# Optimization experiments

Hardware: AMD Instinct MI355X
Metric: run time of the kernel (lower is better)

The kernel has to match this reference:

```python
import jax, jax.numpy as jnp
import numpy as np

N_HEAD = 16
MASKED_BIAS = -10000.0


def setup_inputs() -> dict:
    key = jax.random.key(0)
    k1, k2, k3 = jax.random.split(key, 3)
    B, S, D = 2, 2048, 1024
    scale_in = 0.02  # GPT-2 style init scale for weights
    return {
        "hidden_states": jax.random.normal(k1, (B, S, D), dtype=jnp.float32),
        "c_attn_w": jax.random.normal(k2, (D, 3 * D), dtype=jnp.float32) * scale_in,
        "c_attn_b": jnp.zeros((3 * D,), dtype=jnp.float32),
        "c_proj_w": jax.random.normal(k3, (D, D), dtype=jnp.float32) * scale_in,
        "c_proj_b": jnp.zeros((D,), dtype=jnp.float32),
    }


def reference(hidden_states, c_attn_w, c_attn_b, c_proj_w, c_proj_b):
    B, S, D = hidden_states.shape
    H = N_HEAD
    hd = D // H

    # Conv1D (HF): x @ W + b, fused QKV
    qkv = hidden_states @ c_attn_w + c_attn_b          # [B, S, 3D]
    q, k, v = jnp.split(qkv, 3, axis=-1)

    def to_heads(x):  # [B, S, D] -> [B, H, S, hd]
        return x.reshape(B, S, H, hd).transpose(0, 2, 1, 3)

    q, k, v = to_heads(q), to_heads(k), to_heads(v)

    # scaled scores (scale=True divides by sqrt(head_dim))
    w = jnp.einsum("bhqd,bhkd->bhqk", q, k) / jnp.float32(hd) ** 0.5  # [B,H,S,S]

    # causal mask via torch.where(mask, w, masked_bias)
    causal = jnp.tril(jnp.ones((S, S), dtype=bool))
    w = jnp.where(causal, w, jnp.float32(MASKED_BIAS))

    w = jax.nn.softmax(w, axis=-1)
    # attn_dropout / resid_dropout are identity in eval mode

    out = jnp.einsum("bhqk,bhkd->bhqd", w, v)          # [B,H,S,hd]
    out = out.transpose(0, 2, 1, 3).reshape(B, S, D)   # merge heads

    return out @ c_proj_w + c_proj_b                   # [B,S,D]
```

## Files before the change

kernel.cpp:

```cpp
#include <hip/hip_runtime.h>
#include <hip/hip_bf16.h>

typedef __attribute__((ext_vector_type(8))) short bf16x8;
typedef __attribute__((ext_vector_type(4))) float f32x4;
typedef __attribute__((ext_vector_type(4))) unsigned u32x4;

#define B_SZ 2
#define S_SZ 2048
#define D_SZ 1024
#define H_SZ 16
#define HD_SZ 64

static __device__ __forceinline__ short f2bf(float f) {
    unsigned u = __builtin_bit_cast(unsigned, f);
    u += 0x7FFFu + ((u >> 16) & 1u);
    return (short)(u >> 16);
}

static __device__ __forceinline__ float fexp2(float x) {
    float r; asm("v_exp_f32 %0, %1" : "=v"(r) : "v"(x)); return r;
}

static __device__ __forceinline__ unsigned cvtpk(float lo, float hi) {
    unsigned r; asm("v_cvt_pk_bf16_f32 %0, %1, %2" : "=v"(r) : "v"(lo), "v"(hi)); return r;
}

static __device__ __forceinline__ void gload16(const short* g, short* l) {
    __builtin_amdgcn_global_load_lds(
        (const __attribute__((address_space(1))) unsigned*)g,
        (__attribute__((address_space(3))) unsigned*)l,
        16, 0, 0);
}

#define SBAR() do { __builtin_amdgcn_sched_barrier(0); \
                    __builtin_amdgcn_s_barrier(); \
                    __builtin_amdgcn_sched_barrier(0); } while (0)

__global__ __launch_bounds__(256) void k_prep(const float* __restrict__ hs, short* __restrict__ Xb,
                                              const float* __restrict__ w1, short* __restrict__ W1T,
                                              const float* __restrict__ w2, short* __restrict__ W2T) {
    __shared__ float tile[32][33];
    const int id = blockIdx.x;
    const int tid = threadIdx.x;
    if (id < 4096) {
        int i = (id * 256 + tid) * 4;
        float4 v = *reinterpret_cast<const float4*>(hs + i);
        short4 o;
        o.x = f2bf(v.x); o.y = f2bf(v.y); o.z = f2bf(v.z); o.w = f2bf(v.w);
        *reinterpret_cast<short4*>(Xb + i) = o;
        return;
    }
    const float* in;
    short* out;
    int N, bx, by;
    if (id < 7168) {
        int bid = id - 4096;
        in = w1; out = W1T; N = 3072;
        bx = bid % 96; by = bid / 96;
    } else {
        int bid = id - 7168;
        in = w2; out = W2T; N = 1024;
        bx = bid & 31; by = bid >> 5;
    }
    const int k0 = by * 32, n0 = bx * 32;
    const int tx = tid & 31, ty = tid >> 5;
    #pragma unroll
    for (int i = 0; i < 4; ++i)
        tile[ty + i * 8][tx] = in[(size_t)(k0 + ty + i * 8) * N + n0 + tx];
    __syncthreads();
    #pragma unroll
    for (int i = 0; i < 4; ++i)
        out[(size_t)(n0 + ty + i * 8) * 1024 + k0 + tx] = f2bf(tile[tx][ty + i * 8]);
}

__global__ __launch_bounds__(512, 1) void k_gemm_qkv8(
    const short* __restrict__ A, const short* __restrict__ Bt,
    const float* __restrict__ bias,
    short* __restrict__ Qo, short* __restrict__ Ko, short* __restrict__ VTo) {
    constexpr int K = 1024, NT = 16;
    __shared__ short As[2][256 * 64];
    __shared__ short Bs[2][192 * 64];
    const int tid = threadIdx.x;
    const int lane = tid & 63;
    const int w = tid >> 6;
    const int wr = w >> 2, wc = w & 3;
    const int lr = lane & 15, lc = lane >> 4;
    const int bid = blockIdx.x;
    const int xcd = bid & 7, local = bid >> 3;
    const int bm = (xcd >> 1) * 4 + (local >> 3);
    const int bn = (xcd & 1) * 8 + (local & 7);
    const size_t arow0 = (size_t)bm * 256;
    const size_t brow0 = (size_t)bn * 192;

    const int srl = tid >> 3;
    const int sc8 = (tid & 7) ^ (srl & 7);
    const int dcol = (tid & 7) * 8;

    f32x4 acc[8][3];
    #pragma unroll
    for (int m = 0; m < 8; ++m)
        #pragma unroll
        for (int n = 0; n < 3; ++n)
            acc[m][n] = (f32x4){0.f, 0.f, 0.f, 0.f};

    auto STAGE_A = [&](int T) {
        const int buf = T & 1;
        #pragma unroll
        for (int j = 0; j < 4; ++j) {
            int row = j * 64 + srl;
            gload16(&A[(arow0 + row) * K + T * 64 + sc8 * 8], &As[buf][row * 64 + dcol]);
        }
    };
    auto STAGE_B = [&](int T) {
        const int buf = T & 1;
        #pragma unroll
        for (int j = 0; j < 3; ++j) {
            int row = j * 64 + srl;
            gload16(&Bt[(brow0 + row) * K + T * 64 + sc8 * 8], &Bs[buf][row * 64 + dcol]);
        }
    };

    const int rx = (lr & 7) * 8;
    auto LDA = [&](int buf, int rowoff, int c) {
        return *reinterpret_cast<const bf16x8*>(
            &As[buf][(wr * 128 + rowoff + lr) * 64 + (((c * 32) + lc * 8) ^ rx)]);
    };
    auto LDB = [&](int buf, int n, int c) {
        return *reinterpret_cast<const bf16x8*>(
            &Bs[buf][(wc * 48 + n * 16 + lr) * 64 + (((c * 32) + lc * 8) ^ rx)]);
    };

    bf16x8 at[4][2];
    bf16x8 bfr[3][2];

    STAGE_A(0); STAGE_B(0); STAGE_B(1);
    asm volatile("s_waitcnt vmcnt(3)" ::: "memory");
    SBAR();

    for (int T = 0; T < NT; ++T) {
        const int buf = T & 1;
        #pragma unroll
        for (int m = 0; m < 4; ++m)
            #pragma unroll
            for (int c = 0; c < 2; ++c)
                at[m][c] = LDA(buf, m * 16, c);
        #pragma unroll
        for (int n = 0; n < 3; ++n)
            #pragma unroll
            for (int c = 0; c < 2; ++c)
                bfr[n][c] = LDB(buf, n, c);
        if (T + 1 < NT) STAGE_A(T + 1);
        SBAR();
        __builtin_amdgcn_s_setprio(1);
        #pragma unroll
        for (int m = 0; m < 4; ++m)
            #pragma unroll
            for (int n = 0; n < 3; ++n)
                #pragma unroll
                for (int c = 0; c < 2; ++c)
                    acc[m][n] = __builtin_amdgcn_mfma_f32_16x16x32_bf16(at[m][c], bfr[n][c], acc[m][n], 0, 0, 0);
        __builtin_amdgcn_s_setprio(0);
        SBAR();
        #pragma unroll
        for (int m = 0; m < 4; ++m)
            #pragma unroll
            for (int c = 0; c < 2; ++c)
                at[m][c] = LDA(buf, 64 + m * 16, c);
        if (T + 2 < NT) {
            STAGE_B(T + 2);
            asm volatile("s_waitcnt vmcnt(3)" ::: "memory");
        } else {
            asm volatile("s_waitcnt vmcnt(0)" ::: "memory");
        }
        SBAR();
        __builtin_amdgcn_s_setprio(1);
        #pragma unroll
        for (int m = 0; m < 4; ++m)
            #pragma unroll
            for (int n = 0; n < 3; ++n)
                #pragma unroll
                for (int c = 0; c < 2; ++c)
                    acc[4 + m][n] = __builtin_amdgcn_mfma_f32_16x16x32_bf16(at[m][c], bfr[n][c], acc[4 + m][n], 0, 0, 0);
        __builtin_amdgcn_s_setprio(0);
        SBAR();
    }

    #pragma unroll
    for (int n = 0; n < 3; ++n) {
        const int col = bn * 192 + wc * 48 + n * 16 + lr;
        const float bv = bias[col];
        if (col < 2048) {
            const bool isq = (col < 1024);
            const float scale = isq ? 0.18033688011112042f : 1.0f;
            short* dst = isq ? Qo : Ko;
            const int dg = col & 1023;
            const int hh = dg >> 6, dd = dg & 63;
            #pragma unroll
            for (int m = 0; m < 8; ++m) {
                #pragma unroll
                for (int r = 0; r < 4; ++r) {
                    int grow = bm * 256 + wr * 128 + m * 16 + lc * 4 + r;
                    int b = grow >> 11, s = grow & 2047;
                    dst[(((size_t)(b * H_SZ + hh)) * S_SZ + s) * HD_SZ + dd] = f2bf((acc[m][n][r] + bv) * scale);
                }
            }
        } else {
            const int dv = col - 2048;
            const int hh = dv >> 6, dt = dv & 63;
            #pragma unroll
            for (int m = 0; m < 8; ++m) {
                int grow = bm * 256 + wr * 128 + m * 16 + lc * 4;
                int b = grow >> 11, s = grow & 2047;
                short4 st;
                st.x = f2bf(acc[m][n][0] + bv);
                st.y = f2bf(acc[m][n][1] + bv);
                st.z = f2bf(acc[m][n][2] + bv);
                st.w = f2bf(acc[m][n][3] + bv);
                *reinterpret_cast<short4*>(
                    &VTo[(((size_t)(b * H_SZ + hh)) * HD_SZ + dt) * S_SZ + s]) = st;
            }
        }
    }
}

__global__ __launch_bounds__(256) void k_attn(const short* __restrict__ Q,
                                              const short* __restrict__ Kv,
                                              const short* __restrict__ VT,
                                              short* __restrict__ O) {
    __shared__ short Ks[2][64 * 64];
    __shared__ short Vs[2][64 * 64];
    const int id = blockIdx.x;
    const int bh = ((id & 7) << 2) | ((id >> 3) & 3);
    const int h = bh & 15;
    const int bb = bh >> 4;
    const int g = id >> 5, oct = g >> 3, gr = g & 7;
    const int qt = (oct == 0) ? 31 - gr : (oct == 1) ? 16 + gr : (oct == 2) ? 15 - gr : gr;
    const int tid = threadIdx.x;
    const int lane = tid & 63, w = tid >> 6;
    const int lr = lane & 15, lc = lane >> 4;
    const int qrow0 = qt * 64 + w * 16;
    const size_t base = (size_t)bh * S_SZ * HD_SZ;

    bf16x8 qf[2];
    #pragma unroll
    for (int c = 0; c < 2; ++c)
        qf[c] = *reinterpret_cast<const bf16x8*>(&Q[base + (size_t)(qrow0 + lr) * HD_SZ + c * 32 + lc * 8]);

    float l_run = 0.f;
    f32x4 o_acc[4];
    #pragma unroll
    for (int n = 0; n < 4; ++n) o_acc[n] = (f32x4){0.f, 0.f, 0.f, 0.f};

    const int srow = tid >> 3;
    const int sslot = (tid & 7) ^ (srow & 7);
    const short* kp = &Kv[base + (size_t)srow * HD_SZ + sslot * 8];
    const short* vp = &VT[base + (size_t)srow * S_SZ + sslot * 8];
    auto STAGE = [&](int b) {
        gload16(kp, &Ks[b][tid * 8]);
        gload16(kp + 2048, &Ks[b][2048 + tid * 8]);
        gload16(vp, &Vs[b][tid * 8]);
        gload16(vp + 32 * S_SZ, &Vs[b][2048 + tid * 8]);
        kp += 4096; vp += 64;
    };

    const int q_row = qrow0 + lr;
    const int rxa = (lr & 7) * 8;
    const bool b0 = (lane & 16) != 0;
    const bool b1 = (lane & 32) != 0;

    STAGE(0);
    asm volatile("s_waitcnt vmcnt(0)" ::: "memory");
    SBAR();

    for (int kt = 0; kt <= qt; ++kt) {
        const int buf = kt & 1;
        if (kt < qt) STAGE(buf ^ 1);
        {
            f32x4 sf[4];
            #pragma unroll
            for (int n = 0; n < 4; ++n) {
                f32x4 z = (f32x4){0.f, 0.f, 0.f, 0.f};
                #pragma unroll
                for (int c = 0; c < 2; ++c) {
                    bf16x8 kf = *reinterpret_cast<const bf16x8*>(
                        &Ks[buf][(n * 16 + lr) * 64 + ((c * 32 + lc * 8) ^ rxa)]);
                    z = __builtin_amdgcn_mfma_f32_16x16x32_bf16(kf, qf[c], z, 0, 0, 0);
                }
                sf[n] = z;
            }
            if (kt == qt) {
                const int kb = kt * 64 + lc * 4 - q_row;
                #pragma unroll
                for (int n = 0; n < 4; ++n)
                    #pragma unroll
                    for (int r = 0; r < 4; ++r)
                        sf[n][r] = (kb + n * 16 + r > 0) ? -14427.0f : sf[n][r];
            }
            float rs = 0.f;
            #pragma unroll
            for (int n = 0; n < 4; ++n)
                #pragma unroll
                for (int r = 0; r < 4; ++r) {
                    float pv = fexp2(sf[n][r]);
                    sf[n][r] = pv;
                    rs += pv;
                }
            l_run += rs;
            unsigned Apk0 = cvtpk(sf[0][0], sf[0][1]), Apk1 = cvtpk(sf[0][2], sf[0][3]);
            unsigned Bpk0 = cvtpk(sf[1][0], sf[1][1]), Bpk1 = cvtpk(sf[1][2], sf[1][3]);
            unsigned Cpk0 = cvtpk(sf[2][0], sf[2][1]), Cpk1 = cvtpk(sf[2][2], sf[2][3]);
            unsigned Dpk0 = cvtpk(sf[3][0], sf[3][1]), Dpk1 = cvtpk(sf[3][2], sf[3][3]);
            unsigned x0 = __shfl_xor(b0 ? Apk0 : Bpk0, 16);
            unsigned x1 = __shfl_xor(b0 ? Apk1 : Bpk1, 16);
            unsigned x2 = __shfl_xor(b0 ? Cpk0 : Dpk0, 16);
            unsigned x3 = __shfl_xor(b0 ? Cpk1 : Dpk1, 16);
            unsigned y0 = __shfl_xor(b1 ? Apk0 : Bpk0, 32);
            unsigned y1 = __shfl_xor(b1 ? Apk1 : Bpk1, 32);
            unsigned y2 = __shfl_xor(b1 ? Cpk0 : Dpk0, 32);
            unsigned y3 = __shfl_xor(b1 ? Cpk1 : Dpk1, 32);
            unsigned z0 = __shfl_xor(b1 ? Apk0 : Bpk0, 48);
            unsigned z1 = __shfl_xor(b1 ? Apk1 : Bpk1, 48);
            unsigned z2 = __shfl_xor(b1 ? Cpk0 : Dpk0, 48);
            unsigned z3 = __shfl_xor(b1 ? Cpk1 : Dpk1, 48);
            u32x4 pv0 = { b1 ? (b0 ? x0 : y0) : (b0 ? z0 : Apk0),
                          b1 ? (b0 ? x1 : y1) : (b0 ? z1 : Apk1),
                          b1 ? (b0 ? Bpk0 : z0) : (b0 ? y0 : x0),
                          b1 ? (b0 ? Bpk1 : z1) : (b0 ? y1 : x1) };
            u32x4 pv1 = { b1 ? (b0 ? x2 : y2) : (b0 ? z2 : Cpk0),
                          b1 ? (b0 ? x3 : y3) : (b0 ? z3 : Cpk1),
                          b1 ? (b0 ? Dpk0 : z2) : (b0 ? y2 : x2),
                          b1 ? (b0 ? Dpk1 : z3) : (b0 ? y3 : x3) };
            bf16x8 paA = __builtin_bit_cast(bf16x8, pv0);
            bf16x8 paB = __builtin_bit_cast(bf16x8, pv1);
            #pragma unroll
            for (int c = 0; c < 2; ++c) {
                bf16x8 pa = c ? paB : paA;
                #pragma unroll
                for (int n = 0; n < 4; ++n) {
                    bf16x8 vf = *reinterpret_cast<const bf16x8*>(
                        &Vs[buf][(n * 16 + lr) * 64 + ((c * 32 + lc * 8) ^ rxa)]);
                    o_acc[n] = __builtin_amdgcn_mfma_f32_16x16x32_bf16(pa, vf, o_acc[n], 0, 0, 0);
                }
            }
        }
        asm volatile("s_waitcnt vmcnt(0)" ::: "memory");
        SBAR();
    }

    l_run += __shfl_xor(l_run, 16);
    l_run += __shfl_xor(l_run, 32);
    float li[4];
    #pragma unroll
    for (int r = 0; r < 4; ++r)
        li[r] = 1.0f / __shfl(l_run, lc * 4 + r);
    #pragma unroll
    for (int n = 0; n < 4; ++n) {
        #pragma unroll
        for (int r = 0; r < 4; ++r) {
            float v = o_acc[n][r] * li[r];
            int s = qrow0 + lc * 4 + r;
            O[((size_t)bb * S_SZ + s) * D_SZ + h * 64 + n * 16 + lr] = f2bf(v);
        }
    }
}

__global__ __launch_bounds__(256) void k_gemm_proj(
    const short* __restrict__ A, const short* __restrict__ Bt,
    const float* __restrict__ bias, float* __restrict__ out) {
    constexpr int K = 1024;
    constexpr int N = 1024;
    __shared__ short As[128 * 64];
    __shared__ short Bs[128 * 64];
    const int tid = threadIdx.x;
    const int lane = tid & 63;
    const int w = tid >> 6;
    const int wm = w >> 1, wn = w & 1;
    const int lr = lane & 15, lc = lane >> 4;
    const int bn = blockIdx.x, bm = blockIdx.y;
    const size_t arow0 = (size_t)bm * 128;
    const size_t brow0 = (size_t)bn * 128;

    const short* aptr[4];
    const short* bptr[4];
    short* alds[4];
    short* blds[4];
    #pragma unroll
    for (int i = 0; i < 4; ++i) {
        int cid = w * 4 + i;
        int row = cid * 8 + (lane >> 3);
        int col = (lane & 7) * 8;
        aptr[i] = A + (arow0 + row) * K + col;
        bptr[i] = Bt + (brow0 + row) * K + col;
        alds[i] = &As[cid * 512];
        blds[i] = &Bs[cid * 512];
    }

    f32x4 acc[4][4];
    #pragma unroll
    for (int m = 0; m < 4; ++m)
        #pragma unroll
        for (int n = 0; n < 4; ++n)
            acc[m][n] = (f32x4){0.f, 0.f, 0.f, 0.f};

    for (int kt = 0; kt < K; kt += 64) {
        __syncthreads();
        #pragma unroll
        for (int i = 0; i < 4; ++i) {
            gload16(aptr[i] + kt, alds[i]);
            gload16(bptr[i] + kt, blds[i]);
        }
        __syncthreads();
        #pragma unroll
        for (int c = 0; c < 2; ++c) {
            bf16x8 af[4], bfr[4];
            #pragma unroll
            for (int m = 0; m < 4; ++m)
                af[m] = *reinterpret_cast<const bf16x8*>(&As[(wm * 64 + m * 16 + lr) * 64 + c * 32 + lc * 8]);
            #pragma unroll
            for (int n = 0; n < 4; ++n)
                bfr[n] = *reinterpret_cast<const bf16x8*>(&Bs[(wn * 64 + n * 16 + lr) * 64 + c * 32 + lc * 8]);
            #pragma unroll
            for (int m = 0; m < 4; ++m)
                #pragma unroll
                for (int n = 0; n < 4; ++n)
                    acc[m][n] = __builtin_amdgcn_mfma_f32_16x16x32_bf16(af[m], bfr[n], acc[m][n], 0, 0, 0);
        }
    }

    #pragma unroll
    for (int n = 0; n < 4; ++n) {
        const int col = bn * 128 + wn * 64 + n * 16 + lr;
        const float bv = bias[col];
        #pragma unroll
        for (int m = 0; m < 4; ++m) {
            #pragma unroll
            for (int r = 0; r < 4; ++r) {
                int grow = bm * 128 + wm * 64 + m * 16 + lc * 4 + r;
                out[(size_t)grow * N + col] = acc[m][n][r] + bv;
            }
        }
    }
}

extern "C" void kernel_launch(void* const* d_in, const int* in_sizes, int n_in,
                              void* d_out, int out_size, void* d_ws, size_t ws_size,
                              hipStream_t stream) {
    (void)in_sizes; (void)n_in; (void)out_size; (void)ws_size;
    const float* hs     = (const float*)d_in[0];
    const float* w_attn = (const float*)d_in[1];
    const float* b_attn = (const float*)d_in[2];
    const float* w_proj = (const float*)d_in[3];
    const float* b_proj = (const float*)d_in[4];
    float* out = (float*)d_out;
    char* ws = (char*)d_ws;

    short* Xb  = (short*)(ws + 0);
    short* W1T = (short*)(ws + 8388608);
    short* W2T = (short*)(ws + 14680064);
    short* Qb  = (short*)(ws + 16777216);
    short* Kb  = (short*)(ws + 25165824);
    short* VTb = (short*)(ws + 33554432);
    short* Ob  = (short*)(ws + 0);

    k_prep<<<dim3(8192), dim3(256), 0, stream>>>(hs, Xb, w_attn, W1T, w_proj, W2T);
    k_gemm_qkv8<<<dim3(256), dim3(512), 0, stream>>>(Xb, W1T, b_attn, Qb, Kb, VTb);
    k_attn<<<dim3(1024), dim3(256), 0, stream>>>(Qb, Kb, VTb, Ob);
    k_gemm_proj<<<dim3(8, 32), dim3(256), 0, stream>>>(Ob, W2T, b_proj, out);
}
```

Before: 110.4 us.

## Triple-buffer attention K/V tiles and software-pipeline projection GEMM with swizzled LDS

The attention kernel moves from double to triple buffering of K/V tiles, prefetching two tiles ahead with partial vmcnt waits so global loads overlap more compute. The projection GEMM is rewritten with double-buffered, XOR-swizzled LDS tiles, staggered A/B staging, split MFMA phases with s_setprio, and an XCD-aware block mapping that runs on a 1D grid. The aim is to hide global-load latency, cut LDS bank conflicts, and improve L2 locality. In exchange it uses more LDS per block, which may lower occupancy, and adds more barriers per iteration.

```diff
diff --git a/kernel.cpp b/kernel.cpp
--- a/kernel.cpp
+++ b/kernel.cpp
@@ -227,8 +227,8 @@
                                               const short* __restrict__ Kv,
                                               const short* __restrict__ VT,
                                               short* __restrict__ O) {
-    __shared__ short Ks[2][64 * 64];
-    __shared__ short Vs[2][64 * 64];
+    __shared__ short Ks[3][64 * 64];
+    __shared__ short Vs[3][64 * 64];
     const int id = blockIdx.x;
     const int bh = ((id & 7) << 2) | ((id >> 3) & 3);
     const int h = bh & 15;
@@ -269,12 +269,17 @@
     const bool b1 = (lane & 32) != 0;
 
     STAGE(0);
-    asm volatile("s_waitcnt vmcnt(0)" ::: "memory");
+    if (qt >= 1) {
+        STAGE(1);
+        asm volatile("s_waitcnt vmcnt(4)" ::: "memory");
+    } else {
+        asm volatile("s_waitcnt vmcnt(0)" ::: "memory");
+    }
     SBAR();
 
+    int bufc = 0, stc = 2;
     for (int kt = 0; kt <= qt; ++kt) {
-        const int buf = kt & 1;
-        if (kt < qt) STAGE(buf ^ 1);
+        if (kt + 2 <= qt) STAGE(stc);
         {
             f32x4 sf[4];
             #pragma unroll
@@ -283,7 +288,7 @@
                 #pragma unroll
                 for (int c = 0; c < 2; ++c) {
                     bf16x8 kf = *reinterpret_cast<const bf16x8*>(
-                        &Ks[buf][(n * 16 + lr) * 64 + ((c * 32 + lc * 8) ^ rxa)]);
+                        &Ks[bufc][(n * 16 + lr) * 64 + ((c * 32 + lc * 8) ^ rxa)]);
                     z = __builtin_amdgcn_mfma_f32_16x16x32_bf16(kf, qf[c], z, 0, 0, 0);
                 }
                 sf[n] = z;
@@ -338,13 +343,18 @@
                 #pragma unroll
                 for (int n = 0; n < 4; ++n) {
                     bf16x8 vf = *reinterpret_cast<const bf16x8*>(
-                        &Vs[buf][(n * 16 + lr) * 64 + ((c * 32 + lc * 8) ^ rxa)]);
+                        &Vs[bufc][(n * 16 + lr) * 64 + ((c * 32 + lc * 8) ^ rxa)]);
                     o_acc[n] = __builtin_amdgcn_mfma_f32_16x16x32_bf16(pa, vf, o_acc[n], 0, 0, 0);
                 }
             }
         }
-        asm volatile("s_waitcnt vmcnt(0)" ::: "memory");
-        SBAR();
+        if (kt < qt) {
+            if (kt + 2 <= qt) asm volatile("s_waitcnt vmcnt(4)" ::: "memory");
+            else              asm volatile("s_waitcnt vmcnt(0)" ::: "memory");
+            SBAR();
+        }
+        bufc = (bufc == 2) ? 0 : bufc + 1;
+        stc  = (stc == 2) ? 0 : stc + 1;
     }
 
     l_run += __shfl_xor(l_run, 16);
@@ -364,36 +374,27 @@
     }
 }
 
-__global__ __launch_bounds__(256) void k_gemm_proj(
+__global__ __launch_bounds__(256, 2) void k_gemm_proj(
     const short* __restrict__ A, const short* __restrict__ Bt,
     const float* __restrict__ bias, float* __restrict__ out) {
-    constexpr int K = 1024;
-    constexpr int N = 1024;
-    __shared__ short As[128 * 64];
-    __shared__ short Bs[128 * 64];
+    constexpr int K = 1024, NT = 16, N = 1024;
+    __shared__ short As[2][128 * 64];
+    __shared__ short Bs[2][128 * 64];
     const int tid = threadIdx.x;
     const int lane = tid & 63;
     const int w = tid >> 6;
-    const int wm = w >> 1, wn = w & 1;
+    const int wr = w >> 1, wc = w & 1;
     const int lr = lane & 15, lc = lane >> 4;
-    const int bn = blockIdx.x, bm = blockIdx.y;
+    const int bid = blockIdx.x;
+    const int xcd = bid & 7, local = bid >> 3;
+    const int bm = xcd * 4 + (local & 3);
+    const int bn = local >> 2;
     const size_t arow0 = (size_t)bm * 128;
     const size_t brow0 = (size_t)bn * 128;
 
-    const short* aptr[4];
-    const short* bptr[4];
-    short* alds[4];
-    short* blds[4];
-    #pragma unroll
-    for (int i = 0; i < 4; ++i) {
-        int cid = w * 4 + i;
-        int row = cid * 8 + (lane >> 3);
-        int col = (lane & 7) * 8;
-        aptr[i] = A + (arow0 + row) * K + col;
-        bptr[i] = Bt + (brow0 + row) * K + col;
-        alds[i] = &As[cid * 512];
-        blds[i] = &Bs[cid * 512];
-    }
+    const int srl = tid >> 3;
+    const int sc8 = (tid & 7) ^ (srl & 7);
+    const int dcol = (tid & 7) * 8;
 
     f32x4 acc[4][4];
     #pragma unroll
@@ -402,40 +403,97 @@
         for (int n = 0; n < 4; ++n)
             acc[m][n] = (f32x4){0.f, 0.f, 0.f, 0.f};
 
-    for (int kt = 0; kt < K; kt += 64) {
-        __syncthreads();
-        #pragma unroll
-        for (int i = 0; i < 4; ++i) {
-            gload16(aptr[i] + kt, alds[i]);
-            gload16(bptr[i] + kt, blds[i]);
-        }
-        __syncthreads();
-        #pragma unroll
-        for (int c = 0; c < 2; ++c) {
-            bf16x8 af[4], bfr[4];
-            #pragma unroll
-            for (int m = 0; m < 4; ++m)
-                af[m] = *reinterpret_cast<const bf16x8*>(&As[(wm * 64 + m * 16 + lr) * 64 + c * 32 + lc * 8]);
+    auto STAGE_A = [&](int T) {
+        const int buf = T & 1;
+        #pragma unroll
+        for (int j = 0; j < 4; ++j) {
+            int row = j * 32 + srl;
+            gload16(&A[(arow0 + row) * K + T * 64 + sc8 * 8], &As[buf][row * 64 + dcol]);
+        }
+    };
+    auto STAGE_B = [&](int T) {
+        const int buf = T & 1;
+        #pragma unroll
+        for (int j = 0; j < 4; ++j) {
+            int row = j * 32 + srl;
+            gload16(&Bt[(brow0 + row) * K + T * 64 + sc8 * 8], &Bs[buf][row * 64 + dcol]);
+        }
+    };
+
+    const int rx = (lr & 7) * 8;
+    auto LDA = [&](int buf, int rowoff, int c) {
+        return *reinterpret_cast<const bf16x8*>(
+            &As[buf][(wr * 64 + rowoff + lr) * 64 + (((c * 32) + lc * 8) ^ rx)]);
+    };
+    auto LDB = [&](int buf, int n, int c) {
+        return *reinterpret_cast<const bf16x8*>(
+            &Bs[buf][(wc * 64 + n * 16 + lr) * 64 + (((c * 32) + lc * 8) ^ rx)]);
+    };
+
+    bf16x8 at[2][2];
+    bf16x8 bfr[4][2];
+
+    STAGE_A(0); STAGE_B(0); STAGE_B(1);
+    asm volatile("s_waitcnt vmcnt(4)" ::: "memory");
+    SBAR();
+
+    for (int T = 0; T < NT; ++T) {
+        const int buf = T & 1;
+        #pragma unroll
+        for (int m = 0; m < 2; ++m)
+            #pragma unroll
+            for (int c = 0; c < 2; ++c)
+                at[m][c] = LDA(buf, m * 16, c);
+        #pragma unroll
+        for (int n = 0; n < 4; ++n)
+            #pragma unroll
+            for (int c = 0; c < 2; ++c)
+                bfr[n][c] = LDB(buf, n, c);
+        if (T + 1 < NT) STAGE_A(T + 1);
+        SBAR();
+        __builtin_amdgcn_s_setprio(1);
+        #pragma unroll
+        for (int m = 0; m < 2; ++m)
             #pragma unroll
             for (int n = 0; n < 4; ++n)
-                bfr[n] = *reinterpret_cast<const bf16x8*>(&Bs[(wn * 64 + n * 16 + lr) * 64 + c * 32 + lc * 8]);
-            #pragma unroll
-            for (int m = 0; m < 4; ++m)
-                #pragma unroll
-                for (int n = 0; n < 4; ++n)
-                    acc[m][n] = __builtin_amdgcn_mfma_f32_16x16x32_bf16(af[m], bfr[n], acc[m][n], 0, 0, 0);
-        }
+                #pragma unroll
+                for (int c = 0; c < 2; ++c)
+                    acc[m][n] = __builtin_amdgcn_mfma_f32_16x16x32_bf16(at[m][c], bfr[n][c], acc[m][n], 0, 0, 0);
+        __builtin_amdgcn_s_setprio(0);
+        SBAR();
+        #pragma unroll
+        for (int m = 0; m < 2; ++m)
+            #pragma unroll
+            for (int c = 0; c < 2; ++c)
+                at[m][c] = LDA(buf, 32 + m * 16, c);
+        if (T + 2 < NT) {
+            STAGE_B(T + 2);
+            asm volatile("s_waitcnt vmcnt(4)" ::: "memory");
+        } else {
+            asm volatile("s_waitcnt vmcnt(0)" ::: "memory");
+        }
+        SBAR();
+        __builtin_amdgcn_s_setprio(1);
+        #pragma unroll
+        for (int m = 0; m < 2; ++m)
+            #pragma unroll
+            for (int n = 0; n < 4; ++n)
+                #pragma unroll
+                for (int c = 0; c < 2; ++c)
+                    acc[2 + m][n] = __builtin_amdgcn_mfma_f32_16x16x32_bf16(at[m][c], bfr[n][c], acc[2 + m][n], 0, 0, 0);
+        __builtin_amdgcn_s_setprio(0);
+        SBAR();
     }
 
     #pragma unroll
     for (int n = 0; n < 4; ++n) {
-        const int col = bn * 128 + wn * 64 + n * 16 + lr;
+        const int col = bn * 128 + wc * 64 + n * 16 + lr;
         const float bv = bias[col];
         #pragma unroll
         for (int m = 0; m < 4; ++m) {
             #pragma unroll
             for (int r = 0; r < 4; ++r) {
-                int grow = bm * 128 + wm * 64 + m * 16 + lc * 4 + r;
+                int grow = bm * 128 + wr * 64 + m * 16 + lc * 4 + r;
                 out[(size_t)grow * N + col] = acc[m][n][r] + bv;
             }
         }
@@ -465,5 +523,5 @@
     k_prep<<<dim3(8192), dim3(256), 0, stream>>>(hs, Xb, w_attn, W1T, w_proj, W2T);
     k_gemm_qkv8<<<dim3(256), dim3(512), 0, stream>>>(Xb, W1T, b_attn, Qb, Kb, VTb);
     k_attn<<<dim3(1024), dim3(256), 0, stream>>>(Qb, Kb, VTb, Ob);
-    k_gemm_proj<<<dim3(8, 32), dim3(256), 0, stream>>>(Ob, W2T, b_proj, out);
-}
+    k_gemm_proj<<<dim3(256), dim3(256), 0, stream>>>(Ob, W2T, b_proj, out);
+}
```

After: 97.62 us, median of 2. 1.13x faster.
